# Performance work log

Measured on AMD Instinct MI355X. Metric: run time of the kernel, lower is better.

The kernel has to match this reference:

```python
import jax, jax.numpy as jnp
import numpy as np

B, N, K, H = 8, 3072, 20, 64
NT = B * N            # 24576 total nodes
E = NT * 20           # 491520 GAT edges
HEADS = 4
BN_EPS = 1e-5


def setup_inputs() -> dict:
    key = jax.random.key(0)
    ks = jax.random.split(key, 16)
    rn = lambda k, shp, s=0.05: jax.random.normal(k, shp, dtype=jnp.float32) * s
    z = lambda shp: jnp.zeros(shp, dtype=jnp.float32)
    inp = {}
    inp["x"] = jax.random.normal(ks[0], (NT, 8), dtype=jnp.float32)
    inp["batch"] = jnp.repeat(jnp.arange(B, dtype=jnp.int32), N)
    inp["edge_index"] = jax.random.randint(ks[1], (2, E), 0, NT)
    # lc_encode: Linear(8,32) -> ELU -> Linear(32,H) -> ELU
    inp["enc_W1"] = rn(ks[2], (8, 32)); inp["enc_b1"] = z(32)
    inp["enc_W2"] = rn(ks[3], (32, H)); inp["enc_b2"] = z(H)
    # 3 DynamicEdgeConv MLPs: Linear(2H,H) -> ELU -> BatchNorm(eval) -> Dropout(eval=id)
    inp["conv_W"] = rn(ks[4], (3, 2 * H, H)); inp["conv_b"] = z((3, H))
    inp["bn_g"] = jnp.ones((3, H), jnp.float32); inp["bn_b"] = z((3, H))
    inp["bn_m"] = z((3, H)); inp["bn_v"] = jnp.ones((3, H), jnp.float32)
    # 2 GATConv layers: heads=4, concat=False (mean over heads)
    inp["gat_W"] = rn(ks[5], (2, H, HEADS * H))
    inp["gat_asrc"] = rn(ks[6], (2, HEADS, H))
    inp["gat_adst"] = rn(ks[7], (2, HEADS, H))
    inp["gat_bias"] = z((2, H))
    # output MLP: Linear(H,64) ELU Linear(64,32) ELU Linear(32,8)
    inp["out_W1"] = rn(ks[8], (H, 64)); inp["out_b1"] = z(64)
    inp["out_W2"] = rn(ks[9], (64, 32)); inp["out_b2"] = z(32)
    inp["out_W3"] = rn(ks[10], (32, 8)); inp["out_b3"] = z(8)
    return inp


def _knn_idx(x):
    # x: [B,N,H]; k nearest neighbors per graph, excluding self
    sq = jnp.sum(x * x, axis=-1)
    d = sq[:, :, None] + sq[:, None, :] - 2.0 * jnp.einsum('bnh,bmh->bnm', x, x)
    d = d + jnp.eye(N, dtype=x.dtype)[None] * 1e9
    _, idx = jax.lax.top_k(-d, K)
    return idx  # [B,N,K]


def _dyn_edge_conv(x, W, b, g, be, m, v):
    # x: [B,N,H]; EdgeConv message nn([x_i, x_j - x_i]), max-aggr over k neighbors
    idx = _knn_idx(x)
    xj = jax.vmap(lambda xb, ib: xb[ib])(x, idx)          # [B,N,K,H]
    xi = x[:, :, None, :]
    e = jnp.concatenate([jnp.broadcast_to(xi, xj.shape), xj - xi], axis=-1)  # [B,N,K,2H]
    h = jax.nn.elu(jnp.einsum('bnkf,fh->bnkh', e, W) + b)
    h = g * (h - m) * jax.lax.rsqrt(v + BN_EPS) + be      # BatchNorm1d (eval)
    return jnp.max(h, axis=2)                             # [B,N,H]


def _gat(x, ei, W, asrc, adst, bias):
    # x: [NT,H]; PyG GATConv, heads=4, concat=False, with self-loops
    xh = (x @ W).reshape(NT, HEADS, H)
    loops = jnp.arange(NT)
    src = jnp.concatenate([ei[0], loops])
    dst = jnp.concatenate([ei[1], loops])
    al_s = jnp.einsum('nhc,hc->nh', xh, asrc)
    al_d = jnp.einsum('nhc,hc->nh', xh, adst)
    alpha = jax.nn.leaky_relu(al_s[src] + al_d[dst], 0.2)  # [E+NT, HEADS]
    mx = jax.ops.segment_max(alpha, dst, num_segments=NT)
    ea = jnp.exp(alpha - mx[dst])
    den = jax.ops.segment_sum(ea, dst, num_segments=NT)
    a = ea / (den[dst] + 1e-16)
    out = jax.ops.segment_sum(xh[src] * a[:, :, None], dst, num_segments=NT)
    return out.mean(axis=1) + bias                        # concat=False -> head mean


def reference(x, batch, edge_index, enc_W1, enc_b1, enc_W2, enc_b2,
              conv_W, conv_b, bn_g, bn_b, bn_m, bn_v,
              gat_W, gat_asrc, gat_adst, gat_bias,
              out_W1, out_b1, out_W2, out_b2, out_W3, out_b3):
    # lc_encode (dropout layers are identity in eval mode)
    h = jax.nn.elu(jax.nn.elu(x @ enc_W1 + enc_b1) @ enc_W2 + enc_b2)
    hb = h.reshape(B, N, H)  # regular batch: node i belongs to graph i // N
    for i in range(3):
        hb = _dyn_edge_conv(hb, conv_W[i], conv_b[i], bn_g[i], bn_b[i], bn_m[i], bn_v[i]) + hb
    feats = hb.reshape(NT, H)
    x1 = _gat(feats, edge_index, gat_W[0], gat_asrc[0], gat_adst[0], gat_bias[0]) + feats
    x2 = _gat(x1, edge_index, gat_W[1], gat_asrc[1], gat_adst[1], gat_bias[1]) + x1
    o = jax.nn.elu(x2 @ out_W1 + out_b1)
    o = jax.nn.elu(o @ out_W2 + out_b2)
    return o @ out_W3 + out_b3  # [NT, contrastive_dim]
```

## Files before the change

### kernel.cpp

```cpp
#include <hip/hip_runtime.h>
#include <math.h>

#define NTOT  24576
#define NB    8
#define NPB   3072
#define HD    64
#define KNN   20

__device__ __forceinline__ float elu_f(float x){ return x > 0.f ? x : expm1f(x); }

__global__ __launch_bounds__(256) void enc_kernel(const float* __restrict__ x,
    const float* __restrict__ W1, const float* __restrict__ b1,
    const float* __restrict__ W2, const float* __restrict__ b2,
    float* __restrict__ out){
  __shared__ float sW1[256], sb1[32], sW2[2048], sb2[64];
  int t = threadIdx.x;
  if (t < 256) sW1[t] = W1[t];
  for (int i = t; i < 2048; i += 256) sW2[i] = W2[i];
  if (t < 32) sb1[t] = b1[t];
  if (t < 64) sb2[t] = b2[t];
  __syncthreads();
  int n = blockIdx.x*256 + t;
  const float4* xp = (const float4*)(x + (size_t)n*8);
  float4 x0 = xp[0], x1 = xp[1];
  float xi[8] = {x0.x,x0.y,x0.z,x0.w,x1.x,x1.y,x1.z,x1.w};
  float h1[32];
  #pragma unroll
  for (int j = 0; j < 32; j++){
    float a = sb1[j];
    #pragma unroll
    for (int d = 0; d < 8; d++) a = fmaf(xi[d], sW1[d*32+j], a);
    h1[j] = elu_f(a);
  }
  float4* op = (float4*)(out + (size_t)n*64);
  #pragma unroll
  for (int c4 = 0; c4 < 16; c4++){
    float a0 = sb2[c4*4+0], a1 = sb2[c4*4+1], a2 = sb2[c4*4+2], a3 = sb2[c4*4+3];
    #pragma unroll
    for (int d = 0; d < 32; d++){
      float hd = h1[d];
      float4 wv = *(const float4*)&sW2[d*64 + c4*4];
      a0 = fmaf(hd, wv.x, a0); a1 = fmaf(hd, wv.y, a1);
      a2 = fmaf(hd, wv.z, a2); a3 = fmaf(hd, wv.w, a3);
    }
    float4 o; o.x=elu_f(a0); o.y=elu_f(a1); o.z=elu_f(a2); o.w=elu_f(a3);
    op[c4] = o;
  }
}

__global__ __launch_bounds__(256) void sq_kernel(const float* __restrict__ f, float* __restrict__ sq){
  int n = blockIdx.x*256 + threadIdx.x;
  const float4* p = (const float4*)(f + (size_t)n*64);
  float s = 0.f;
  #pragma unroll
  for (int i = 0; i < 16; i++){
    float4 v = p[i];
    s = fmaf(v.x,v.x,s); s = fmaf(v.y,v.y,s); s = fmaf(v.z,v.z,s); s = fmaf(v.w,v.w,s);
  }
  sq[n] = s;
}

__global__ __launch_bounds__(256) void dist_kernel(const float* __restrict__ feat,
    const float* __restrict__ sqn, float* __restrict__ D, int q0, int cq){
  int b  = blockIdx.z;
  int m0 = blockIdx.x * 128;
  int qc0 = blockIdx.y * 128;
  int qg0 = q0 + qc0;
  const float* fb = feat + (size_t)b*NPB*HD;
  float* Db = D + (size_t)b*cq*NPB;
  __shared__ float As[64][128];
  __shared__ float Bs[64][128];
  int t = threadIdx.x;
  {
    int r = t >> 1, dc = (t & 1) * 32;
    const float4* pa = (const float4*)(fb + (size_t)(qg0 + r)*HD + dc);
    const float4* pb = (const float4*)(fb + (size_t)(m0 + r)*HD + dc);
    #pragma unroll
    for (int i = 0; i < 8; i++){
      float4 va = pa[i], vb = pb[i];
      int d = dc + i*4;
      As[d][r]=va.x; As[d+1][r]=va.y; As[d+2][r]=va.z; As[d+3][r]=va.w;
      Bs[d][r]=vb.x; Bs[d+1][r]=vb.y; Bs[d+2][r]=vb.z; Bs[d+3][r]=vb.w;
    }
  }
  __syncthreads();
  int tx = t & 15, ty = t >> 4;
  float acc[8][8];
  #pragma unroll
  for (int i = 0; i < 8; i++)
    #pragma unroll
    for (int j = 0; j < 8; j++) acc[i][j] = 0.f;
  #pragma unroll 2
  for (int d = 0; d < 64; d++){
    float af[8], bf[8];
    *(float4*)&af[0] = *(const float4*)&As[d][ty*8];
    *(float4*)&af[4] = *(const float4*)&As[d][ty*8+4];
    *(float4*)&bf[0] = *(const float4*)&Bs[d][tx*8];
    *(float4*)&bf[4] = *(const float4*)&Bs[d][tx*8+4];
    #pragma unroll
    for (int i = 0; i < 8; i++)
      #pragma unroll
      for (int j = 0; j < 8; j++)
        acc[i][j] = fmaf(af[i], bf[j], acc[i][j]);
  }
  const float4* sp = (const float4*)(sqn + (size_t)b*NPB + m0 + tx*8);
  float4 sq0 = sp[0], sq1 = sp[1];
  float sqv[8] = {sq0.x,sq0.y,sq0.z,sq0.w,sq1.x,sq1.y,sq1.z,sq1.w};
  #pragma unroll
  for (int i = 0; i < 8; i++){
    float* orow = Db + (size_t)(qc0 + ty*8 + i)*NPB + m0 + tx*8;
    float4 o0, o1;
    o0.x = fmaf(-2.f, acc[i][0], sqv[0]); o0.y = fmaf(-2.f, acc[i][1], sqv[1]);
    o0.z = fmaf(-2.f, acc[i][2], sqv[2]); o0.w = fmaf(-2.f, acc[i][3], sqv[3]);
    o1.x = fmaf(-2.f, acc[i][4], sqv[4]); o1.y = fmaf(-2.f, acc[i][5], sqv[5]);
    o1.z = fmaf(-2.f, acc[i][6], sqv[6]); o1.w = fmaf(-2.f, acc[i][7], sqv[7]);
    *(float4*)orow = o0; *((float4*)orow + 1) = o1;
  }
}

__global__ __launch_bounds__(256) void select_kernel(const float* __restrict__ D,
    int* __restrict__ idxout, int q0, int cq){
  __shared__ float srows[4][3072];
  __shared__ float cvs[4][72];
  __shared__ int   cxs[4][72];
  int wid = threadIdx.x >> 6;
  int w = blockIdx.x*4 + wid;
  int lane = threadIdx.x & 63;
  int b  = w / cq;
  int qc = w - b*cq;
  int ql = q0 + qc;
  int g  = b*NPB + ql;
  const float* row = D + ((size_t)b*cq + qc) * NPB;
  const float INF = 3.4e38f;
  int qh = ql >> 8, qlw = (ql >> 2) & 63, qe = ql & 3;
  bool dlane = (qlw == lane);
  float* srow = srows[wid];
  float a1 = INF;
  #pragma unroll
  for (int c = 0; c < 12; c++){
    float4 vv = *(const float4*)(row + c*256 + lane*4);
    if (dlane && (qh == c)){
      if      (qe == 0) vv.x = INF;
      else if (qe == 1) vv.y = INF;
      else if (qe == 2) vv.z = INF;
      else              vv.w = INF;
    }
    *(float4*)&srow[c*256 + lane*4] = vv;
    a1 = fminf(a1, fminf(fminf(vv.x, vv.y), fminf(vv.z, vv.w)));
  }
  {
    float v = a1;
    #pragma unroll
    for (int k = 2; k <= 64; k <<= 1){
      #pragma unroll
      for (int j = k >> 1; j > 0; j >>= 1){
        float o = __shfl_xor(v, j, 64);
        bool up    = ((lane & k) == 0);
        bool lower = ((lane & j) == 0);
        float mn = fminf(v, o), mx = fmaxf(v, o);
        v = (lower == up) ? mn : mx;
      }
    }
    a1 = __shfl(v, 19, 64);
  }
  float T = a1;
  float* cv = cvs[wid];
  int*   cx = cxs[wid];
  int base = 0;
  #pragma unroll
  for (int c = 0; c < 12; c++){
    float4 vv = *(const float4*)&srow[c*256 + lane*4];
    #pragma unroll
    for (int e = 0; e < 4; e++){
      float s = (e==0)?vv.x:(e==1)?vv.y:(e==2)?vv.z:vv.w;
      bool fire = (s <= T);
      unsigned long long mk = __ballot(fire);
      if (mk){
        int pos = base + (int)__popcll(mk & ((1ull << lane) - 1ull));
        if (fire && pos < 64){ cv[pos] = s; cx[pos] = c*256 + lane*4 + e; }
        base += (int)__popcll(mk);
      }
    }
  }
  if (base <= 64){
    unsigned long long key;
    if (lane < base){
      unsigned int ku = __float_as_uint(cv[lane]);
      ku ^= (unsigned)(((int)ku) >> 31) | 0x80000000u;
      key = ((unsigned long long)ku << 32) | (unsigned int)cx[lane];
    } else key = ~0ull;
    #pragma unroll
    for (int k = 2; k <= 64; k <<= 1){
      #pragma unroll
      for (int j = k >> 1; j > 0; j >>= 1){
        unsigned long long o = __shfl_xor(key, j, 64);
        bool up    = ((lane & k) == 0);
        bool lower = ((lane & j) == 0);
        unsigned long long mn = key < o ? key : o;
        unsigned long long mx = key < o ? o : key;
        key = (lower == up) ? mn : mx;
      }
    }
    if (lane < KNN)
      idxout[(size_t)g*KNN + lane] = b*NPB + (int)(unsigned int)(key & 0xffffffffu);
  } else {
    float dl[KNN]; int il[KNN];
    #pragma unroll
    for (int k = 0; k < KNN; k++){ dl[k] = INF; il[k] = 0x7fffffff; }
    #pragma unroll 1
    for (int c = 0; c < 12; c++){
      float4 vv = *(const float4*)&srow[c*256 + lane*4];
      #pragma unroll
      for (int e = 0; e < 4; e++){
        float s = (e==0)?vv.x:(e==1)?vv.y:(e==2)?vv.z:vv.w;
        int m = c*256 + lane*4 + e;
        if (s < dl[KNN-1]){
          #pragma unroll
          for (int k = KNN-1; k >= 1; k--){
            bool c1 = s < dl[k-1];
            bool c0 = s < dl[k];
            dl[k] = c1 ? dl[k-1] : (c0 ? s : dl[k]);
            il[k] = c1 ? il[k-1] : (c0 ? m : il[k]);
          }
          if (s < dl[0]){ dl[0] = s; il[0] = m; }
        }
      }
    }
    int res = 0;
    #pragma unroll 1
    for (int r = 0; r < KNN; r++){
      float d = dl[0]; int i = il[0];
      #pragma unroll
      for (int off = 1; off < 64; off <<= 1){
        float od = __shfl_xor(d, off, 64);
        int   oi = __shfl_xor(i, off, 64);
        if (od < d || (od == d && oi < i)){ d = od; i = oi; }
      }
      if (lane == r) res = i;
      if (il[0] == i){
        #pragma unroll
        for (int k = 0; k < KNN-1; k++){ dl[k] = dl[k+1]; il[k] = il[k+1]; }
        dl[KNN-1] = INF; il[KNN-1] = 0x7fffffff;
      }
    }
    if (lane < KNN) idxout[(size_t)g*KNN + lane] = b*NPB + res;
  }
}

__global__ __launch_bounds__(256) void knn_kernel(const float* __restrict__ feat,
    const float* __restrict__ sqn, int* __restrict__ idxout){
  int b  = blockIdx.x / 48;
  int q0 = (blockIdx.x % 48) * 64;
  int t  = threadIdx.x;
  int ty = t >> 4, tx = t & 15;
  __shared__ float As[64][64];
  __shared__ float Bs[64][64];
  __shared__ float Ds[64][68];
  __shared__ float ssq[64];
  const float* fb = feat + (size_t)b*NPB*HD;
  {
    int r = t >> 2, dc = (t & 3)*16;
    const float4* src = (const float4*)(fb + (size_t)(q0 + r)*HD + dc);
    #pragma unroll
    for (int i = 0; i < 4; i++){
      float4 v = src[i]; int d = dc + i*4;
      As[d][r]=v.x; As[d+1][r]=v.y; As[d+2][r]=v.z; As[d+3][r]=v.w;
    }
  }
  float dist[KNN]; int didx[KNN];
  #pragma unroll
  for (int i = 0; i < KNN; i++){ dist[i] = 3.4e38f; didx[i] = 0; }
  int qloc = q0 + t;
  for (int m0 = 0; m0 < NPB; m0 += 64){
    __syncthreads();
    {
      int r = t >> 2, dc = (t & 3)*16;
      const float4* src = (const float4*)(fb + (size_t)(m0 + r)*HD + dc);
      #pragma unroll
      for (int i = 0; i < 4; i++){
        float4 v = src[i]; int d = dc + i*4;
        Bs[d][r]=v.x; Bs[d+1][r]=v.y; Bs[d+2][r]=v.z; Bs[d+3][r]=v.w;
      }
      if (t < 64) ssq[t] = sqn[(size_t)b*NPB + m0 + t];
    }
    __syncthreads();
    float acc[4][4];
    #pragma unroll
    for (int i = 0; i < 4; i++)
      #pragma unroll
      for (int j = 0; j < 4; j++) acc[i][j] = 0.f;
    #pragma unroll 4
    for (int d = 0; d < 64; d++){
      float4 av = *(const float4*)&As[d][ty*4];
      float4 bv = *(const float4*)&Bs[d][tx*4];
      acc[0][0]=fmaf(av.x,bv.x,acc[0][0]); acc[0][1]=fmaf(av.x,bv.y,acc[0][1]);
      acc[0][2]=fmaf(av.x,bv.z,acc[0][2]); acc[0][3]=fmaf(av.x,bv.w,acc[0][3]);
      acc[1][0]=fmaf(av.y,bv.x,acc[1][0]); acc[1][1]=fmaf(av.y,bv.y,acc[1][1]);
      acc[1][2]=fmaf(av.y,bv.z,acc[1][2]); acc[1][3]=fmaf(av.y,bv.w,acc[1][3]);
      acc[2][0]=fmaf(av.z,bv.x,acc[2][0]); acc[2][1]=fmaf(av.z,bv.y,acc[2][1]);
      acc[2][2]=fmaf(av.z,bv.z,acc[2][2]); acc[2][3]=fmaf(av.z,bv.w,acc[2][3]);
      acc[3][0]=fmaf(av.w,bv.x,acc[3][0]); acc[3][1]=fmaf(av.w,bv.y,acc[3][1]);
      acc[3][2]=fmaf(av.w,bv.z,acc[3][2]); acc[3][3]=fmaf(av.w,bv.w,acc[3][3]);
    }
    #pragma unroll
    for (int i = 0; i < 4; i++){
      float4 o; o.x=acc[i][0]; o.y=acc[i][1]; o.z=acc[i][2]; o.w=acc[i][3];
      *(float4*)&Ds[ty*4+i][tx*4] = o;
    }
    __syncthreads();
    if (t < 64){
      #pragma unroll 1
      for (int j = 0; j < 64; j++){
        int m = m0 + j;
        float s = fmaf(-2.f, Ds[t][j], ssq[j]);
        if (m == qloc) continue;
        if (s < dist[KNN-1]){
          #pragma unroll
          for (int k = KNN-1; k >= 1; k--){
            bool sh = s < dist[k-1];
            float nd = sh ? dist[k-1] : (s < dist[k] ? s : dist[k]);
            int   ni = sh ? didx[k-1] : (s < dist[k] ? m : didx[k]);
            dist[k] = nd; didx[k] = ni;
          }
          if (s < dist[0]){ dist[0] = s; didx[0] = m; }
        }
      }
    }
  }
  if (t < 64){
    int* op = idxout + (size_t)((size_t)b*NPB + q0 + t)*KNN;
    #pragma unroll
    for (int k = 0; k < KNN; k++) op[k] = b*NPB + didx[k];
  }
}

__global__ __launch_bounds__(256) void uv_kernel(const float* __restrict__ feat,
    const float* __restrict__ W, const float* __restrict__ cb,
    float* __restrict__ u, float* __restrict__ v){
  __shared__ float sW[128*64];
  int t = threadIdx.x;
  for (int i = t; i < 8192; i += 256) sW[i] = W[i];
  __syncthreads();
  int n = blockIdx.x*256 + t;
  float4 fv[16];
  const float4* fp = (const float4*)(feat + (size_t)n*64);
  #pragma unroll
  for (int i = 0; i < 16; i++) fv[i] = fp[i];
  float4* up = (float4*)(u + (size_t)n*64);
  float4* vp = (float4*)(v + (size_t)n*64);
  #pragma unroll 1
  for (int c4 = 0; c4 < 16; c4++){
    float ua0=0,ua1=0,ua2=0,ua3=0, vb0=0,vb1=0,vb2=0,vb3=0;
    #pragma unroll
    for (int d4 = 0; d4 < 16; d4++){
      float4 fq = fv[d4];
      #pragma unroll
      for (int dd = 0; dd < 4; dd++){
        int d = d4*4 + dd;
        float fd = dd==0?fq.x : dd==1?fq.y : dd==2?fq.z : fq.w;
        float4 wt = *(const float4*)&sW[d*64 + c4*4];
        float4 wb = *(const float4*)&sW[(64+d)*64 + c4*4];
        ua0=fmaf(fd,wt.x,ua0); ua1=fmaf(fd,wt.y,ua1); ua2=fmaf(fd,wt.z,ua2); ua3=fmaf(fd,wt.w,ua3);
        vb0=fmaf(fd,wb.x,vb0); vb1=fmaf(fd,wb.y,vb1); vb2=fmaf(fd,wb.z,vb2); vb3=fmaf(fd,wb.w,vb3);
      }
    }
    float4 cbv = *(const float4*)&cb[c4*4];
    float4 uo, vo;
    uo.x = cbv.x + ua0 - vb0; uo.y = cbv.y + ua1 - vb1;
    uo.z = cbv.z + ua2 - vb2; uo.w = cbv.w + ua3 - vb3;
    vo.x = vb0; vo.y = vb1; vo.z = vb2; vo.w = vb3;
    up[c4] = uo; vp[c4] = vo;
  }
}

__global__ __launch_bounds__(256) void pool_kernel(const float* __restrict__ u, const float* __restrict__ v,
    const int* __restrict__ idx, const float* __restrict__ resid,
    const float* __restrict__ bg, const float* __restrict__ bb,
    const float* __restrict__ bm, const float* __restrict__ bv,
    float* __restrict__ out){
  int gid = blockIdx.x*256 + threadIdx.x;
  int n = gid >> 6, lane = gid & 63;
  float uc = u[(size_t)n*64 + lane];
  float scale = bg[lane] / sqrtf(bv[lane] + 1e-5f);
  float bias  = bb[lane] - bm[lane]*scale;
  const int* ip = idx + (size_t)n*KNN;
  float acc = -3.4e38f;
  #pragma unroll 4
  for (int k = 0; k < KNN; k++){
    int j = ip[k];
    float s = uc + v[(size_t)j*64 + lane];
    acc = fmaxf(acc, fmaf(elu_f(s), scale, bias));
  }
  out[(size_t)n*64 + lane] = acc + resid[(size_t)n*64 + lane];
}

__global__ void deg_init(int* deg){ int i = blockIdx.x*256 + threadIdx.x; if (i < NTOT) deg[i] = 1; }
__global__ void deg_hist(const int* __restrict__ ei, int E, int* deg){
  int i = blockIdx.x*256 + threadIdx.x; if (i < E) atomicAdd(&deg[ei[E + i]], 1);
}
__global__ void scan_kernel(const int* __restrict__ deg, int* __restrict__ rowptr, int* __restrict__ cursor){
  __shared__ int part[256];
  int t = threadIdx.x;
  int base = t*96;
  int s = 0;
  for (int i = 0; i < 96; i++) s += deg[base + i];
  part[t] = s;
  __syncthreads();
  for (int off = 1; off < 256; off <<= 1){
    int xv = (t >= off) ? part[t - off] : 0;
    __syncthreads();
    part[t] += xv;
    __syncthreads();
  }
  int run = part[t] - s;
  for (int i = 0; i < 96; i++){
    rowptr[base + i] = run; cursor[base + i] = run; run += deg[base + i];
  }
  if (t == 255) rowptr[NTOT] = run;
}
__global__ void scatter_kernel(const int* __restrict__ ei, int E, int* cursor, int* __restrict__ csr){
  int i = blockIdx.x*256 + threadIdx.x;
  if (i >= E + NTOT) return;
  int s, d;
  if (i < E){ s = ei[i]; d = ei[E + i]; } else { s = i - E; d = s; }
  int pos = atomicAdd(&cursor[d], 1);
  csr[pos] = s;
}

__global__ __launch_bounds__(256) void xh_kernel(const float* __restrict__ feat,
    const float* __restrict__ W, const float* __restrict__ asrc, const float* __restrict__ adst,
    float* __restrict__ xh, float* __restrict__ al){
  __shared__ float sW[64*128];
  __shared__ float sas[256], sad[256];
  int t = threadIdx.x;
  if (t < 256){ sas[t] = asrc[t]; sad[t] = adst[t]; }
  int n = blockIdx.x*256 + t;
  float4 fv[16];
  const float4* fp = (const float4*)(feat + (size_t)n*64);
  #pragma unroll
  for (int i = 0; i < 16; i++) fv[i] = fp[i];
  float4* xp = (float4*)(xh + (size_t)n*256);
  float* ap = al + (size_t)n*8;
  #pragma unroll 1
  for (int half = 0; half < 2; half++){
    __syncthreads();
    for (int i = t; i < 8192; i += 256){
      int d = i >> 7, c = i & 127;
      sW[i] = W[d*256 + half*128 + c];
    }
    __syncthreads();
    #pragma unroll 1
    for (int hh = 0; hh < 2; hh++){
      int h = half*2 + hh;
      float as_ = 0.f, ad_ = 0.f;
      #pragma unroll 1
      for (int cc = 0; cc < 64; cc += 4){
        int c  = h*64 + cc;
        int cl = hh*64 + cc;
        float a0=0,a1=0,a2=0,a3=0;
        #pragma unroll
        for (int d4 = 0; d4 < 16; d4++){
          float4 fq = fv[d4];
          #pragma unroll
          for (int dd = 0; dd < 4; dd++){
            int d = d4*4 + dd;
            float fd = dd==0?fq.x : dd==1?fq.y : dd==2?fq.z : fq.w;
            float4 wv = *(const float4*)&sW[d*128 + cl];
            a0=fmaf(fd,wv.x,a0); a1=fmaf(fd,wv.y,a1); a2=fmaf(fd,wv.z,a2); a3=fmaf(fd,wv.w,a3);
          }
        }
        float4 o; o.x=a0; o.y=a1; o.z=a2; o.w=a3;
        xp[c >> 2] = o;
        as_ = fmaf(a0, sas[c], fmaf(a1, sas[c+1], fmaf(a2, sas[c+2], fmaf(a3, sas[c+3], as_))));
        ad_ = fmaf(a0, sad[c], fmaf(a1, sad[c+1], fmaf(a2, sad[c+2], fmaf(a3, sad[c+3], ad_))));
      }
      ap[h] = as_; ap[4 + h] = ad_;
    }
  }
}

__global__ __launch_bounds__(256) void agg_kernel(const float* __restrict__ xh, const float* __restrict__ al,
    const int* __restrict__ rowptr, const int* __restrict__ csr,
    const float* __restrict__ resid, const float* __restrict__ bias,
    float* __restrict__ out){
  int gid = blockIdx.x*256 + threadIdx.x;
  int n = gid >> 6, lane = gid & 63;
  int rs = rowptr[n], re = rowptr[n+1];
  int h = lane >> 4, coff = (lane & 15)*4;
  float ald_h = al[(size_t)n*8 + 4 + h];
  float mx = -3.4e38f, den = 0.f;
  float ax=0.f, ay=0.f, az=0.f, aw=0.f;
  #pragma unroll 2
  for (int e = rs; e < re; e++){
    int s = csr[e];
    float a = al[(size_t)s*8 + h] + ald_h;
    a = a > 0.f ? a : 0.2f*a;
    float nm = fmaxf(mx, a);
    float corr = __expf(mx - nm);
    float ea   = __expf(a - nm);
    mx = nm;
    float4 xv = *(const float4*)(xh + (size_t)s*256 + h*64 + coff);
    den = fmaf(den, corr, ea);
    ax = fmaf(ax, corr, ea*xv.x); ay = fmaf(ay, corr, ea*xv.y);
    az = fmaf(az, corr, ea*xv.z); aw = fmaf(aw, corr, ea*xv.w);
  }
  float rinv = 1.f / (den + 1e-16f);
  float r0 = ax*rinv, r1 = ay*rinv, r2 = az*rinv, r3 = aw*rinv;
  r0 += __shfl_xor(r0, 16, 64); r1 += __shfl_xor(r1, 16, 64);
  r2 += __shfl_xor(r2, 16, 64); r3 += __shfl_xor(r3, 16, 64);
  r0 += __shfl_xor(r0, 32, 64); r1 += __shfl_xor(r1, 32, 64);
  r2 += __shfl_xor(r2, 32, 64); r3 += __shfl_xor(r3, 32, 64);
  if (lane < 16){
    float4 bs = *(const float4*)(bias + coff);
    float4 rv = *(const float4*)(resid + (size_t)n*64 + coff);
    float4 o;
    o.x = r0*0.25f + bs.x + rv.x; o.y = r1*0.25f + bs.y + rv.y;
    o.z = r2*0.25f + bs.z + rv.z; o.w = r3*0.25f + bs.w + rv.w;
    *(float4*)(out + (size_t)n*64 + coff) = o;
  }
}

__global__ __launch_bounds__(256) void mlp_kernel(const float* __restrict__ feat,
    const float* __restrict__ W1, const float* __restrict__ b1,
    const float* __restrict__ W2, const float* __restrict__ b2,
    const float* __restrict__ W3, const float* __restrict__ b3,
    float* __restrict__ out){
  __shared__ float s1[4096], s2[2048], s3[256], t1[64], t2[32], t3[8];
  int t = threadIdx.x;
  for (int i = t; i < 4096; i += 256) s1[i] = W1[i];
  for (int i = t; i < 2048; i += 256) s2[i] = W2[i];
  if (t < 256) s3[t] = W3[t];
  if (t < 64) t1[t] = b1[t];
  if (t < 32) t2[t] = b2[t];
  if (t < 8)  t3[t] = b3[t];
  __syncthreads();
  int n = blockIdx.x*256 + t;
  float4 fv[16];
  const float4* fp = (const float4*)(feat + (size_t)n*64);
  #pragma unroll
  for (int i = 0; i < 16; i++) fv[i] = fp[i];
  float o1[64];
  #pragma unroll 1
  for (int c4 = 0; c4 < 16; c4++){
    float a0=t1[c4*4+0], a1=t1[c4*4+1], a2=t1[c4*4+2], a3=t1[c4*4+3];
    #pragma unroll
    for (int d4 = 0; d4 < 16; d4++){
      float4 fq = fv[d4];
      #pragma unroll
      for (int dd = 0; dd < 4; dd++){
        int d = d4*4 + dd;
        float fd = dd==0?fq.x : dd==1?fq.y : dd==2?fq.z : fq.w;
        float4 wv = *(const float4*)&s1[d*64 + c4*4];
        a0=fmaf(fd,wv.x,a0); a1=fmaf(fd,wv.y,a1); a2=fmaf(fd,wv.z,a2); a3=fmaf(fd,wv.w,a3);
      }
    }
    o1[c4*4+0]=elu_f(a0); o1[c4*4+1]=elu_f(a1); o1[c4*4+2]=elu_f(a2); o1[c4*4+3]=elu_f(a3);
  }
  float o2[32];
  #pragma unroll 1
  for (int c4 = 0; c4 < 8; c4++){
    float a0=t2[c4*4+0], a1=t2[c4*4+1], a2=t2[c4*4+2], a3=t2[c4*4+3];
    #pragma unroll
    for (int d = 0; d < 64; d++){
      float fd = o1[d];
      float4 wv = *(const float4*)&s2[d*32 + c4*4];
      a0=fmaf(fd,wv.x,a0); a1=fmaf(fd,wv.y,a1); a2=fmaf(fd,wv.z,a2); a3=fmaf(fd,wv.w,a3);
    }
    o2[c4*4+0]=elu_f(a0); o2[c4*4+1]=elu_f(a1); o2[c4*4+2]=elu_f(a2); o2[c4*4+3]=elu_f(a3);
  }
  float4* op = (float4*)(out + (size_t)n*8);
  #pragma unroll
  for (int c4 = 0; c4 < 2; c4++){
    float a0=t3[c4*4+0], a1=t3[c4*4+1], a2=t3[c4*4+2], a3=t3[c4*4+3];
    #pragma unroll
    for (int d = 0; d < 32; d++){
      float fd = o2[d];
      float4 wv = *(const float4*)&s3[d*8 + c4*4];
      a0=fmaf(fd,wv.x,a0); a1=fmaf(fd,wv.y,a1); a2=fmaf(fd,wv.z,a2); a3=fmaf(fd,wv.w,a3);
    }
    float4 o; o.x=a0; o.y=a1; o.z=a2; o.w=a3;
    op[c4] = o;
  }
}

extern "C" void kernel_launch(void* const* d_in, const int* in_sizes, int n_in,
                              void* d_out, int out_size, void* d_ws, size_t ws_size,
                              hipStream_t stream){
  (void)n_in; (void)out_size;
  const float* x     = (const float*)d_in[0];
  const int*   ei    = (const int*)d_in[2];
  const int    E     = in_sizes[2] / 2;
  const float* encW1 = (const float*)d_in[3];
  const float* encb1 = (const float*)d_in[4];
  const float* encW2 = (const float*)d_in[5];
  const float* encb2 = (const float*)d_in[6];
  const float* convW = (const float*)d_in[7];
  const float* convb = (const float*)d_in[8];
  const float* bng   = (const float*)d_in[9];
  const float* bnb   = (const float*)d_in[10];
  const float* bnm   = (const float*)d_in[11];
  const float* bnv   = (const float*)d_in[12];
  const float* gatW  = (const float*)d_in[13];
  const float* gatas = (const float*)d_in[14];
  const float* gatad = (const float*)d_in[15];
  const float* gatb  = (const float*)d_in[16];
  const float* oW1   = (const float*)d_in[17];
  const float* ob1   = (const float*)d_in[18];
  const float* oW2   = (const float*)d_in[19];
  const float* ob2   = (const float*)d_in[20];
  const float* oW3   = (const float*)d_in[21];
  const float* ob3   = (const float*)d_in[22];

  char* wp = (char*)d_ws;
  auto alloc = [&](size_t bytes)->void*{
    void* p = (void*)wp; wp += (bytes + 255) & ~((size_t)255); return p;
  };
  float* fA     = (float*)alloc((size_t)NTOT*64*4);
  float* fB     = (float*)alloc((size_t)NTOT*64*4);
  float* ubuf   = (float*)alloc((size_t)NTOT*64*4);
  float* vbuf   = (float*)alloc((size_t)NTOT*64*4);
  float* sqb    = (float*)alloc((size_t)NTOT*4);
  int*   idxb   = (int*)  alloc((size_t)NTOT*KNN*4);
  float* xhb    = (float*)alloc((size_t)NTOT*256*4);
  float* alb    = (float*)alloc((size_t)NTOT*8*4);
  int*   degb   = (int*)  alloc((size_t)NTOT*4);
  int*   rowptr = (int*)  alloc((size_t)(NTOT+1)*4);
  int*   cursor = (int*)  alloc((size_t)NTOT*4);
  int*   csr    = (int*)  alloc((size_t)(E+NTOT)*4);

  size_t used  = (size_t)(wp - (char*)d_ws);
  size_t avail = ws_size > used ? ws_size - used : 0;
  int CQ = (int)(avail / ((size_t)NB * NPB * sizeof(float)));
  CQ = (CQ / 128) * 128;
  if (CQ > NPB) CQ = NPB;
  float* Dbuf = (float*)wp;

  enc_kernel<<<96,256,0,stream>>>(x, encW1, encb1, encW2, encb2, fA);
  float* cur = fA; float* nxt = fB;
  for (int l = 0; l < 3; l++){
    sq_kernel<<<96,256,0,stream>>>(cur, sqb);
    if (CQ >= 128){
      for (int q0 = 0; q0 < NPB; q0 += CQ){
        int cq = NPB - q0 < CQ ? NPB - q0 : CQ;
        dist_kernel  <<<dim3(24, cq/128, NB),256,0,stream>>>(cur, sqb, Dbuf, q0, cq);
        select_kernel<<<(NB*cq)/4,           256,0,stream>>>(Dbuf, idxb, q0, cq);
      }
    } else {
      knn_kernel<<<384,256,0,stream>>>(cur, sqb, idxb);
    }
    uv_kernel  <<<96,  256,0,stream>>>(cur, convW + (size_t)l*8192, convb + l*64, ubuf, vbuf);
    pool_kernel<<<6144,256,0,stream>>>(ubuf, vbuf, idxb, cur,
                                       bng + l*64, bnb + l*64, bnm + l*64, bnv + l*64, nxt);
    float* tmp = cur; cur = nxt; nxt = tmp;
  }
  deg_init   <<<96,            256,0,stream>>>(degb);
  deg_hist   <<<(E+255)/256,   256,0,stream>>>(ei, E, degb);
  scan_kernel<<<1,             256,0,stream>>>(degb, rowptr, cursor);
  scatter_kernel<<<(E+NTOT+255)/256,256,0,stream>>>(ei, E, cursor, csr);
  for (int l = 0; l < 2; l++){
    xh_kernel <<<96,  256,0,stream>>>(cur, gatW + (size_t)l*16384, gatas + l*256, gatad + l*256, xhb, alb);
    agg_kernel<<<6144,256,0,stream>>>(xhb, alb, rowptr, csr, cur, gatb + l*64, nxt);
    float* tmp = cur; cur = nxt; nxt = tmp;
  }
  mlp_kernel<<<96,256,0,stream>>>(cur, oW1, ob1, oW2, ob2, oW3, ob3, (float*)d_out);
}
```

Measured before the change: 1.250 ms.

## Fuse distance tiles with per-tile top-4 and select from candidates

The distance GEMM kernel now keeps its 128x128 tile in shared memory and reduces it to the top-4 candidates per query row, writing only 96 values and byte indices per query. Writing and re-reading the full dense distance matrix in global memory is no longer needed. A new selection kernel finds the 20th-smallest threshold among the candidates and recomputes exact distances for tiles whose 4th candidate still passes the threshold, since those tiles may hold more winners. This adds recomputation work for tiles that overflow and adds shared-memory-bound reduction in the GEMM kernel.

```diff
diff --git a/kernel.cpp b/kernel.cpp
--- a/kernel.cpp
+++ b/kernel.cpp
@@ -6,6 +6,7 @@
 #define NPB   3072
 #define HD    64
 #define KNN   20
+#define NTILE 24
 
 __device__ __forceinline__ float elu_f(float x){ return x > 0.f ? x : expm1f(x); }
 
@@ -60,27 +61,30 @@
   sq[n] = s;
 }
 
-__global__ __launch_bounds__(256) void dist_kernel(const float* __restrict__ feat,
-    const float* __restrict__ sqn, float* __restrict__ D, int q0, int cq){
+#define CE(va,ia,vb,ib) { bool sw_ = (vb) < (va); float t1_ = sw_?(vb):(va); float t2_ = sw_?(va):(vb); int t3_ = sw_?(ib):(ia); int t4_ = sw_?(ia):(ib); (va)=t1_; (vb)=t2_; (ia)=t3_; (ib)=t4_; }
+
+union DSMem {
+  struct { float As[64][128]; float Bs[64][128]; } ab;
+  float Ds[128][129];
+};
+__global__ __launch_bounds__(256) void disttop_kernel(const float* __restrict__ feat,
+    const float* __restrict__ sqn, float* __restrict__ topv, unsigned char* __restrict__ topi){
+  __shared__ DSMem U;
   int b  = blockIdx.z;
   int m0 = blockIdx.x * 128;
-  int qc0 = blockIdx.y * 128;
-  int qg0 = q0 + qc0;
+  int q0 = blockIdx.y * 128;
   const float* fb = feat + (size_t)b*NPB*HD;
-  float* Db = D + (size_t)b*cq*NPB;
-  __shared__ float As[64][128];
-  __shared__ float Bs[64][128];
   int t = threadIdx.x;
   {
     int r = t >> 1, dc = (t & 1) * 32;
-    const float4* pa = (const float4*)(fb + (size_t)(qg0 + r)*HD + dc);
+    const float4* pa = (const float4*)(fb + (size_t)(q0 + r)*HD + dc);
     const float4* pb = (const float4*)(fb + (size_t)(m0 + r)*HD + dc);
     #pragma unroll
     for (int i = 0; i < 8; i++){
       float4 va = pa[i], vb = pb[i];
       int d = dc + i*4;
-      As[d][r]=va.x; As[d+1][r]=va.y; As[d+2][r]=va.z; As[d+3][r]=va.w;
-      Bs[d][r]=vb.x; Bs[d+1][r]=vb.y; Bs[d+2][r]=vb.z; Bs[d+3][r]=vb.w;
+      U.ab.As[d][r]=va.x; U.ab.As[d+1][r]=va.y; U.ab.As[d+2][r]=va.z; U.ab.As[d+3][r]=va.w;
+      U.ab.Bs[d][r]=vb.x; U.ab.Bs[d+1][r]=vb.y; U.ab.Bs[d+2][r]=vb.z; U.ab.Bs[d+3][r]=vb.w;
     }
   }
   __syncthreads();
@@ -93,63 +97,87 @@
   #pragma unroll 2
   for (int d = 0; d < 64; d++){
     float af[8], bf[8];
-    *(float4*)&af[0] = *(const float4*)&As[d][ty*8];
-    *(float4*)&af[4] = *(const float4*)&As[d][ty*8+4];
-    *(float4*)&bf[0] = *(const float4*)&Bs[d][tx*8];
-    *(float4*)&bf[4] = *(const float4*)&Bs[d][tx*8+4];
+    *(float4*)&af[0] = *(const float4*)&U.ab.As[d][ty*8];
+    *(float4*)&af[4] = *(const float4*)&U.ab.As[d][ty*8+4];
+    *(float4*)&bf[0] = *(const float4*)&U.ab.Bs[d][tx*8];
+    *(float4*)&bf[4] = *(const float4*)&U.ab.Bs[d][tx*8+4];
     #pragma unroll
     for (int i = 0; i < 8; i++)
       #pragma unroll
       for (int j = 0; j < 8; j++)
         acc[i][j] = fmaf(af[i], bf[j], acc[i][j]);
   }
-  const float4* sp = (const float4*)(sqn + (size_t)b*NPB + m0 + tx*8);
-  float4 sq0 = sp[0], sq1 = sp[1];
-  float sqv[8] = {sq0.x,sq0.y,sq0.z,sq0.w,sq1.x,sq1.y,sq1.z,sq1.w};
+  float sqv[8];
+  {
+    const float4* sp = (const float4*)(sqn + (size_t)b*NPB + m0 + tx*8);
+    float4 sq0 = sp[0], sq1 = sp[1];
+    sqv[0]=sq0.x; sqv[1]=sq0.y; sqv[2]=sq0.z; sqv[3]=sq0.w;
+    sqv[4]=sq1.x; sqv[5]=sq1.y; sqv[6]=sq1.z; sqv[7]=sq1.w;
+  }
+  __syncthreads();
   #pragma unroll
   for (int i = 0; i < 8; i++){
-    float* orow = Db + (size_t)(qc0 + ty*8 + i)*NPB + m0 + tx*8;
-    float4 o0, o1;
-    o0.x = fmaf(-2.f, acc[i][0], sqv[0]); o0.y = fmaf(-2.f, acc[i][1], sqv[1]);
-    o0.z = fmaf(-2.f, acc[i][2], sqv[2]); o0.w = fmaf(-2.f, acc[i][3], sqv[3]);
-    o1.x = fmaf(-2.f, acc[i][4], sqv[4]); o1.y = fmaf(-2.f, acc[i][5], sqv[5]);
-    o1.z = fmaf(-2.f, acc[i][6], sqv[6]); o1.w = fmaf(-2.f, acc[i][7], sqv[7]);
-    *(float4*)orow = o0; *((float4*)orow + 1) = o1;
-  }
-}
-
-__global__ __launch_bounds__(256) void select_kernel(const float* __restrict__ D,
-    int* __restrict__ idxout, int q0, int cq){
-  __shared__ float srows[4][3072];
+    float* dr = &U.Ds[ty*8+i][tx*8];
+    #pragma unroll
+    for (int j = 0; j < 8; j++) dr[j] = fmaf(-2.f, acc[i][j], sqv[j]);
+  }
+  __syncthreads();
+  const float INF = 3.4e38f;
+  int qr = t >> 1, half = t & 1;
+  int qg = q0 + qr;
+  int cex = qg - m0;
+  float s0=INF,s1=INF,s2=INF,s3=INF;
+  int i0=0,i1=0,i2=0,i3=0;
+  int cbase = half*64;
+  #pragma unroll 8
+  for (int j = 0; j < 64; j++){
+    int c = cbase + j;
+    float v = U.Ds[qr][c];
+    if (c == cex) v = INF;
+    bool l3 = v < s3, l2 = v < s2, l1 = v < s1, l0 = v < s0;
+    s3 = l2 ? s2 : (l3 ? v : s3);  i3 = l2 ? i2 : (l3 ? c : i3);
+    s2 = l1 ? s1 : (l2 ? v : s2);  i2 = l1 ? i1 : (l2 ? c : i2);
+    s1 = l0 ? s0 : (l1 ? v : s1);  i1 = l0 ? i0 : (l1 ? c : i1);
+    s0 = l0 ? v : s0;              i0 = l0 ? c : i0;
+  }
+  float b0 = __shfl_xor(s0,1,64), b1v = __shfl_xor(s1,1,64),
+        b2v = __shfl_xor(s2,1,64), b3v = __shfl_xor(s3,1,64);
+  int  bi0 = __shfl_xor(i0,1,64), bi1 = __shfl_xor(i1,1,64),
+       bi2 = __shfl_xor(i2,1,64), bi3 = __shfl_xor(i3,1,64);
+  bool c0 = s0 <= b3v; float w0 = c0 ? s0 : b3v; int x0 = c0 ? i0 : bi3;
+  bool c1 = s1 <= b2v; float w1 = c1 ? s1 : b2v; int x1 = c1 ? i1 : bi2;
+  bool c2 = s2 <= b1v; float w2 = c2 ? s2 : b1v; int x2 = c2 ? i2 : bi1;
+  bool c3 = s3 <= b0;  float w3 = c3 ? s3 : b0;  int x3 = c3 ? i3 : bi0;
+  CE(w0,x0,w2,x2); CE(w1,x1,w3,x3); CE(w0,x0,w1,x1); CE(w2,x2,w3,x3); CE(w1,x1,w2,x2);
+  if (half == 0){
+    size_t g = (size_t)b*NPB + qg;
+    float4 ov; ov.x=w0; ov.y=w1; ov.z=w2; ov.w=w3;
+    *(float4*)(topv + g*96 + blockIdx.x*4) = ov;
+    uchar4 oi; oi.x=(unsigned char)x0; oi.y=(unsigned char)x1;
+    oi.z=(unsigned char)x2; oi.w=(unsigned char)x3;
+    *(uchar4*)(topi + g*96 + blockIdx.x*4) = oi;
+  }
+}
+
+__global__ __launch_bounds__(256) void ksel_kernel(const float* __restrict__ topv,
+    const unsigned char* __restrict__ topi, const float* __restrict__ feat,
+    const float* __restrict__ sqn, int* __restrict__ idxout){
   __shared__ float cvs[4][72];
   __shared__ int   cxs[4][72];
-  int wid = threadIdx.x >> 6;
-  int w = blockIdx.x*4 + wid;
-  int lane = threadIdx.x & 63;
-  int b  = w / cq;
-  int qc = w - b*cq;
-  int ql = q0 + qc;
-  int g  = b*NPB + ql;
-  const float* row = D + ((size_t)b*cq + qc) * NPB;
+  int wid = threadIdx.x >> 6, lane = threadIdx.x & 63;
+  int g = blockIdx.x*4 + wid;
+  int b = g / NPB;
+  int ql = g - b*NPB;
   const float INF = 3.4e38f;
-  int qh = ql >> 8, qlw = (ql >> 2) & 63, qe = ql & 3;
-  bool dlane = (qlw == lane);
-  float* srow = srows[wid];
-  float a1 = INF;
-  #pragma unroll
-  for (int c = 0; c < 12; c++){
-    float4 vv = *(const float4*)(row + c*256 + lane*4);
-    if (dlane && (qh == c)){
-      if      (qe == 0) vv.x = INF;
-      else if (qe == 1) vv.y = INF;
-      else if (qe == 2) vv.z = INF;
-      else              vv.w = INF;
-    }
-    *(float4*)&srow[c*256 + lane*4] = vv;
-    a1 = fminf(a1, fminf(fminf(vv.x, vv.y), fminf(vv.z, vv.w)));
-  }
+  const float* tv = topv + (size_t)g*96;
+  const unsigned char* ti = topi + (size_t)g*96;
+  float v0 = tv[lane];
+  int   j0 = ti[lane];
+  float v1 = (lane < 32) ? tv[64+lane] : INF;
+  int   j1 = (lane < 32) ? (int)ti[64+lane] : 0;
+  float T;
   {
-    float v = a1;
+    float v = fminf(v0, v1);
     #pragma unroll
     for (int k = 2; k <= 64; k <<= 1){
       #pragma unroll
@@ -161,25 +189,53 @@
         v = (lower == up) ? mn : mx;
       }
     }
-    a1 = __shfl(v, 19, 64);
-  }
-  float T = a1;
-  float* cv = cvs[wid];
-  int*   cx = cxs[wid];
-  int base = 0;
-  #pragma unroll
-  for (int c = 0; c < 12; c++){
-    float4 vv = *(const float4*)&srow[c*256 + lane*4];
-    #pragma unroll
-    for (int e = 0; e < 4; e++){
-      float s = (e==0)?vv.x:(e==1)?vv.y:(e==2)?vv.z:vv.w;
-      bool fire = (s <= T);
-      unsigned long long mk = __ballot(fire);
-      if (mk){
-        int pos = base + (int)__popcll(mk & ((1ull << lane) - 1ull));
-        if (fire && pos < 64){ cv[pos] = s; cx[pos] = c*256 + lane*4 + e; }
-        base += (int)__popcll(mk);
-      }
+    T = __shfl(v, 19, 64);
+  }
+  unsigned long long fb1 = __ballot(((lane & 3) == 3) && (v0 <= T));
+  unsigned long long fb2 = __ballot((lane < 32) && ((lane & 3) == 3) && (v1 <= T));
+  unsigned int flags = 0;
+  #pragma unroll
+  for (int k = 0; k < 16; k++) flags |= (unsigned)((fb1 >> (4*k+3)) & 1ull) << k;
+  #pragma unroll
+  for (int k = 0; k < 8; k++)  flags |= (unsigned)((fb2 >> (4*k+3)) & 1ull) << (16+k);
+  float* cv = cvs[wid]; int* cx = cxs[wid];
+  int t0 = lane >> 2;
+  bool f0 = (v0 <= T) && !((flags >> t0) & 1u);
+  unsigned long long mk = __ballot(f0);
+  int pos = (int)__popcll(mk & ((1ull<<lane)-1ull));
+  if (f0 && pos < 64){ cv[pos] = v0; cx[pos] = t0*128 + j0; }
+  int base = (int)__popcll(mk);
+  int t1 = 16 + (lane >> 2);
+  bool f1 = (lane < 32) && (v1 <= T) && !((flags >> t1) & 1u);
+  mk = __ballot(f1);
+  pos = base + (int)__popcll(mk & ((1ull<<lane)-1ull));
+  if (f1 && pos < 64){ cv[pos] = v1; cx[pos] = t1*128 + j1; }
+  base += (int)__popcll(mk);
+  const float* fqp = feat + (size_t)g*HD;
+  unsigned int fl = flags;
+  while (fl){
+    int tt = __ffs(fl) - 1; fl &= fl - 1;
+    #pragma unroll
+    for (int r = 0; r < 2; r++){
+      int c = r*64 + lane;
+      int m = tt*128 + c;
+      const float* fmp = feat + (size_t)(b*NPB + m)*HD;
+      float acc = 0.f;
+      #pragma unroll
+      for (int d4 = 0; d4 < 16; d4++){
+        float4 fq4 = *(const float4*)(fqp + d4*4);
+        float4 fm4 = *(const float4*)(fmp + d4*4);
+        acc = fmaf(fq4.x, fm4.x, acc);
+        acc = fmaf(fq4.y, fm4.y, acc);
+        acc = fmaf(fq4.z, fm4.z, acc);
+        acc = fmaf(fq4.w, fm4.w, acc);
+      }
+      float s = fmaf(-2.f, acc, sqn[(size_t)b*NPB + m]);
+      bool fire = (m != ql) && (s <= T);
+      unsigned long long mk2 = __ballot(fire);
+      int p2 = base + (int)__popcll(mk2 & ((1ull<<lane)-1ull));
+      if (fire && p2 < 64){ cv[p2] = s; cx[p2] = m; }
+      base += (int)__popcll(mk2);
     }
   }
   if (base <= 64){
@@ -208,22 +264,29 @@
     #pragma unroll
     for (int k = 0; k < KNN; k++){ dl[k] = INF; il[k] = 0x7fffffff; }
     #pragma unroll 1
-    for (int c = 0; c < 12; c++){
-      float4 vv = *(const float4*)&srow[c*256 + lane*4];
-      #pragma unroll
-      for (int e = 0; e < 4; e++){
-        float s = (e==0)?vv.x:(e==1)?vv.y:(e==2)?vv.z:vv.w;
-        int m = c*256 + lane*4 + e;
-        if (s < dl[KNN-1]){
-          #pragma unroll
-          for (int k = KNN-1; k >= 1; k--){
-            bool c1 = s < dl[k-1];
-            bool c0 = s < dl[k];
-            dl[k] = c1 ? dl[k-1] : (c0 ? s : dl[k]);
-            il[k] = c1 ? il[k-1] : (c0 ? m : il[k]);
-          }
-          if (s < dl[0]){ dl[0] = s; il[0] = m; }
+    for (int j = 0; j < 48; j++){
+      int m = j*64 + lane;
+      if (m == ql) continue;
+      const float* fmp = feat + (size_t)(b*NPB + m)*HD;
+      float acc = 0.f;
+      for (int d4 = 0; d4 < 16; d4++){
+        float4 fq4 = *(const float4*)(fqp + d4*4);
+        float4 fm4 = *(const float4*)(fmp + d4*4);
+        acc = fmaf(fq4.x, fm4.x, acc);
+        acc = fmaf(fq4.y, fm4.y, acc);
+        acc = fmaf(fq4.z, fm4.z, acc);
+        acc = fmaf(fq4.w, fm4.w, acc);
+      }
+      float s = fmaf(-2.f, acc, sqn[(size_t)b*NPB + m]);
+      if (s < dl[KNN-1]){
+        #pragma unroll
+        for (int k = KNN-1; k >= 1; k--){
+          bool c1 = s < dl[k-1];
+          bool c0 = s < dl[k];
+          dl[k] = c1 ? dl[k-1] : (c0 ? s : dl[k]);
+          il[k] = c1 ? il[k-1] : (c0 ? m : il[k]);
         }
+        if (s < dl[0]){ dl[0] = s; il[0] = m; }
       }
     }
     int res = 0;
@@ -627,24 +690,19 @@
   int*   rowptr = (int*)  alloc((size_t)(NTOT+1)*4);
   int*   cursor = (int*)  alloc((size_t)NTOT*4);
   int*   csr    = (int*)  alloc((size_t)(E+NTOT)*4);
-
-  size_t used  = (size_t)(wp - (char*)d_ws);
-  size_t avail = ws_size > used ? ws_size - used : 0;
-  int CQ = (int)(avail / ((size_t)NB * NPB * sizeof(float)));
-  CQ = (CQ / 128) * 128;
-  if (CQ > NPB) CQ = NPB;
-  float* Dbuf = (float*)wp;
+  float* topv   = (float*)alloc((size_t)NTOT*96*4);
+  unsigned char* topi = (unsigned char*)alloc((size_t)NTOT*96);
+
+  size_t used = (size_t)(wp - (char*)d_ws);
+  bool fused = (ws_size >= used);
 
   enc_kernel<<<96,256,0,stream>>>(x, encW1, encb1, encW2, encb2, fA);
   float* cur = fA; float* nxt = fB;
   for (int l = 0; l < 3; l++){
     sq_kernel<<<96,256,0,stream>>>(cur, sqb);
-    if (CQ >= 128){
-      for (int q0 = 0; q0 < NPB; q0 += CQ){
-        int cq = NPB - q0 < CQ ? NPB - q0 : CQ;
-        dist_kernel  <<<dim3(24, cq/128, NB),256,0,stream>>>(cur, sqb, Dbuf, q0, cq);
-        select_kernel<<<(NB*cq)/4,           256,0,stream>>>(Dbuf, idxb, q0, cq);
-      }
+    if (fused){
+      disttop_kernel<<<dim3(NTILE,NTILE,NB),256,0,stream>>>(cur, sqb, topv, topi);
+      ksel_kernel   <<<NTOT/4,              256,0,stream>>>(topv, topi, cur, sqb, idxb);
     } else {
       knn_kernel<<<384,256,0,stream>>>(cur, sqb, idxb);
     }
```

Result: slower. 1.502 ms (+20.1%).
